# Kernel optimization log

Measured on AMD Instinct MI355X. Metric: run time of the kernel, lower is better.

## Reference

```python
import jax, jax.numpy as jnp
import numpy as np

N_RES = 768
DISTO_BINS = 64
LDDT_BINS = 50
MIN_RESOLUTION = 0.1
MAX_RESOLUTION = 3.0
W_DISTO, W_PLDDT, W_EXP = 0.3, 0.01, 0.01
CA_IDX = 1  # atom37 index of C-alpha


def setup_inputs() -> dict:
    key = jax.random.key(0)
    ks = jax.random.split(key, 6)
    B = 1
    return {
        "distogram_logits": jax.random.normal(ks[0], (B, N_RES, N_RES, DISTO_BINS), jnp.float32),
        "pseudo_beta": jax.random.normal(ks[1], (B, N_RES, 3), jnp.float32) * 10.0,
        "pseudo_beta_mask": jnp.ones((B, N_RES), jnp.float32),
        "lddt_logits": jax.random.normal(ks[2], (B, N_RES, LDDT_BINS), jnp.float32),
        "all_atom_pred_pos": jax.random.normal(ks[3], (B, N_RES, 37, 3), jnp.float32) * 10.0,
        "all_atom_positions": jax.random.normal(ks[4], (B, N_RES, 37, 3), jnp.float32) * 10.0,
        "all_atom_mask": jnp.ones((B, N_RES, 37), jnp.float32),
        "exp_resolved_logits": jax.random.normal(ks[5], (B, N_RES, 37), jnp.float32),
        "atom37_atom_exists": jnp.ones((B, N_RES, 37), jnp.float32),
        "resolution": jnp.ones((B,), jnp.float32),
    }


def _lddt(pred_pos, true_pos, mask, cutoff=15.0, eps=1e-10):
    # pred_pos/true_pos: [*, N, 3]; mask: [*, N, 1] -> per-residue lddt [*, N]
    n = mask.shape[-2]
    dmat_true = jnp.sqrt(eps + jnp.sum((true_pos[..., :, None, :] - true_pos[..., None, :, :]) ** 2, axis=-1))
    dmat_pred = jnp.sqrt(eps + jnp.sum((pred_pos[..., :, None, :] - pred_pos[..., None, :, :]) ** 2, axis=-1))
    scope = ((dmat_true < cutoff).astype(dmat_true.dtype)
             * mask * jnp.swapaxes(mask, -1, -2)
             * (1.0 - jnp.eye(n, dtype=dmat_true.dtype)))
    dist_l1 = jnp.abs(dmat_true - dmat_pred)
    score = 0.25 * ((dist_l1 < 0.5).astype(dist_l1.dtype) + (dist_l1 < 1.0)
                    + (dist_l1 < 2.0) + (dist_l1 < 4.0))
    norm = 1.0 / (eps + jnp.sum(scope, axis=-1))
    return norm * (eps + jnp.sum(scope * score, axis=-1))


def _ce_from_bins(logits, bins):
    # -sum(one_hot(bins) * log_softmax(logits)) == -log_softmax gathered at bins
    logp = jax.nn.log_softmax(logits, axis=-1)
    return -jnp.take_along_axis(logp, bins[..., None], axis=-1)[..., 0]


def _distogram_loss(logits, pseudo_beta, pseudo_beta_mask,
                    min_bin=2.3125, max_bin=21.6875, no_bins=DISTO_BINS, eps=1e-6):
    boundaries = jnp.linspace(min_bin, max_bin, no_bins - 1) ** 2
    d2 = jnp.sum((pseudo_beta[..., :, None, :] - pseudo_beta[..., None, :, :]) ** 2,
                 axis=-1, keepdims=True)  # [*, N, N, 1]
    true_bins = jnp.sum(d2 > boundaries, axis=-1).astype(jnp.int32)  # [*, N, N]
    errors = _ce_from_bins(logits, true_bins)
    sq_mask = pseudo_beta_mask[..., None] * pseudo_beta_mask[..., None, :]
    denom = eps + jnp.sum(sq_mask, axis=(-1, -2))
    mean = jnp.sum(errors * sq_mask, axis=-1) / denom[..., None]
    return jnp.mean(jnp.sum(mean, axis=-1))


def _lddt_loss(logits, all_atom_pred_pos, all_atom_positions, all_atom_mask, resolution,
               no_bins=LDDT_BINS, eps=1e-10):
    pred_ca = all_atom_pred_pos[..., CA_IDX, :]
    true_ca = all_atom_positions[..., CA_IDX, :]
    mask_ca = all_atom_mask[..., CA_IDX:CA_IDX + 1]  # [*, N, 1]
    score = jax.lax.stop_gradient(_lddt(pred_ca, true_ca, mask_ca, eps=eps))
    bin_idx = jnp.clip(jnp.floor(score * no_bins).astype(jnp.int32), 0, no_bins - 1)
    errors = _ce_from_bins(logits, bin_idx)
    m = mask_ca[..., 0]
    loss = jnp.sum(errors * m, axis=-1) / (eps + jnp.sum(m, axis=-1))
    gate = ((resolution >= MIN_RESOLUTION) & (resolution <= MAX_RESOLUTION)).astype(loss.dtype)
    return jnp.mean(loss * gate)


def _exp_resolved_loss(logits, atom37_atom_exists, all_atom_mask, resolution, eps=1e-8):
    errors = (-all_atom_mask * jax.nn.log_sigmoid(logits)
              - (1.0 - all_atom_mask) * jax.nn.log_sigmoid(-logits))
    loss = jnp.sum(errors * atom37_atom_exists, axis=-1)  # [*, N]
    loss = loss / (eps + jnp.sum(atom37_atom_exists, axis=(-1, -2)))[..., None]
    loss = jnp.sum(loss, axis=-1)
    gate = ((resolution >= MIN_RESOLUTION) & (resolution <= MAX_RESOLUTION)).astype(loss.dtype)
    return jnp.mean(loss * gate)


def reference(distogram_logits, pseudo_beta, pseudo_beta_mask, lddt_logits,
              all_atom_pred_pos, all_atom_positions, all_atom_mask,
              exp_resolved_logits, atom37_atom_exists, resolution):
    l_disto = _distogram_loss(distogram_logits, pseudo_beta, pseudo_beta_mask)
    l_plddt = _lddt_loss(lddt_logits, all_atom_pred_pos, all_atom_positions,
                         all_atom_mask, resolution)
    l_exp = _exp_resolved_loss(exp_resolved_logits, atom37_atom_exists,
                               all_atom_mask, resolution)
    return W_DISTO * l_disto + W_PLDDT * l_plddt + W_EXP * l_exp
```

## Files before the change

### kernel.cpp

```cpp
#include <hip/hip_runtime.h>
#include <math.h>

#define N_RES 768
#define DISTO_BINS 64
#define LDDT_BINS 50
#define DISTO_GRID 2048
#define EXP_GRID 64
#define NPAIRS (N_RES * N_RES)
#define NCHUNKS (NPAIRS / 4)

#define ROW_ADD_ROR(v, N)                                                     \
    v += __int_as_float(__builtin_amdgcn_update_dpp(                          \
        0, __float_as_int(v), 0x120 | (N), 0xF, 0xF, false))

__global__ __launch_bounds__(256)
void pair_meta_kernel(const float* __restrict__ pb,
                      const float* __restrict__ pbm,
                      unsigned char* __restrict__ bins,
                      float* __restrict__ wgt) {
    int p = blockIdx.x * blockDim.x + threadIdx.x;
    if (p >= NPAIRS) return;
    int i = p / N_RES;
    int j = p - i * N_RES;
    float dx = pb[3 * i + 0] - pb[3 * j + 0];
    float dy = pb[3 * i + 1] - pb[3 * j + 1];
    float dz = pb[3 * i + 2] - pb[3 * j + 2];
    float d  = sqrtf(dx * dx + dy * dy + dz * dz);
    float t  = ceilf((d - 2.3125f) * 3.2f);
    int bin  = (int)fminf(fmaxf(t, 0.f), 63.f);
    bins[p]  = (unsigned char)bin;
    wgt[p]   = pbm[i] * pbm[j];
}

__global__ __launch_bounds__(256)
void disto_partial_kernel(const float4* __restrict__ logits4,
                          const unsigned int* __restrict__ binw,
                          const float* __restrict__ wgt,
                          float* __restrict__ partial) {
    const int lane = threadIdx.x & 63;
    const int wid  = threadIdx.x >> 6;
    const int q    = lane >> 4;
    const int gl   = lane & 15;
    const int gw   = blockIdx.x * 4 + wid;
    const int nw   = DISTO_GRID * 4;

    float acc = 0.f;

#define DISTO_PROC(xv4, cc)                                                   \
    {                                                                         \
        float e = __expf(xv4.x) + __expf(xv4.y) + __expf(xv4.z) +             \
                  __expf(xv4.w);                                              \
        ROW_ADD_ROR(e, 8);                                                    \
        ROW_ADD_ROR(e, 4);                                                    \
        ROW_ADD_ROR(e, 2);                                                    \
        ROW_ADD_ROR(e, 1);                                                    \
        unsigned int bw = binw[cc];                                           \
        int bin = (int)((bw >> (q * 8)) & 63u);                               \
        float w  = wgt[(cc) * 4 + q];                                         \
        float xs = (bin & 2) ? ((bin & 1) ? xv4.w : xv4.z)                    \
                             : ((bin & 1) ? xv4.y : xv4.x);                   \
        float lg = (gl == 0) ? w * __logf(e) : 0.f;                           \
        float bt = (gl == (bin >> 2)) ? w * xs : 0.f;                         \
        acc += lg - bt;                                                       \
    }

    for (int c0 = gw; c0 < NCHUNKS; c0 += 4 * nw) {
        const int c1 = c0 + nw;
        const int c2 = c0 + 2 * nw;
        const int c3 = c0 + 3 * nw;
        float4 x0 = logits4[(size_t)c0 * 64 + lane];
        float4 x1 = (c1 < NCHUNKS) ? logits4[(size_t)c1 * 64 + lane]
                                   : make_float4(0.f, 0.f, 0.f, 0.f);
        float4 x2 = (c2 < NCHUNKS) ? logits4[(size_t)c2 * 64 + lane]
                                   : make_float4(0.f, 0.f, 0.f, 0.f);
        float4 x3 = (c3 < NCHUNKS) ? logits4[(size_t)c3 * 64 + lane]
                                   : make_float4(0.f, 0.f, 0.f, 0.f);

        DISTO_PROC(x0, c0);
        if (c1 < NCHUNKS) DISTO_PROC(x1, c1);
        if (c2 < NCHUNKS) DISTO_PROC(x2, c2);
        if (c3 < NCHUNKS) DISTO_PROC(x3, c3);
    }
#undef DISTO_PROC

    acc += __shfl_xor(acc, 1, 64);
    acc += __shfl_xor(acc, 2, 64);
    acc += __shfl_xor(acc, 4, 64);
    acc += __shfl_xor(acc, 8, 64);
    acc += __shfl_xor(acc, 16, 64);
    acc += __shfl_xor(acc, 32, 64);
    __shared__ float wsum[4];
    if (lane == 0) wsum[wid] = acc;
    __syncthreads();
    if (threadIdx.x == 0)
        partial[blockIdx.x] = wsum[0] + wsum[1] + wsum[2] + wsum[3];
}

__global__ __launch_bounds__(128)
void small_losses_kernel(const float* __restrict__ pred37,
                         const float* __restrict__ true37,
                         const float* __restrict__ mask37,
                         const float* __restrict__ lddt_logits,
                         const float* __restrict__ exl,
                         const float* __restrict__ a37ex,
                         float* __restrict__ errm,
                         float* __restrict__ expnum,
                         float* __restrict__ expden) {
    const int tid  = threadIdx.x;
    const int nthr = blockDim.x;
    __shared__ float r1[128], r2[128];

    if (blockIdx.x >= N_RES) {
        const int b = blockIdx.x - N_RES;
        const int gid = b * nthr + tid;
        const int stride = EXP_GRID * nthr;
        const int n = N_RES * 37;
        float num = 0.f, den = 0.f;
        for (int k = gid; k < n; k += stride) {
            float x  = exl[k];
            float m  = mask37[k];
            float ex = a37ex[k];
            float ax = fabsf(x);
            float sp = __logf(1.f + __expf(-ax));
            float ls  = sp + fmaxf(-x, 0.f);
            float lsn = sp + fmaxf(x, 0.f);
            float err = m * ls + (1.f - m) * lsn;
            num += err * ex;
            den += ex;
        }
        r1[tid] = num;
        r2[tid] = den;
        __syncthreads();
        for (int s = nthr >> 1; s > 0; s >>= 1) {
            if (tid < s) { r1[tid] += r1[tid + s]; r2[tid] += r2[tid + s]; }
            __syncthreads();
        }
        if (tid == 0) { expnum[b] = r1[0]; expden[b] = r2[0]; }
        return;
    }

    const int i = blockIdx.x;
    const float tix = true37[(i * 37 + 1) * 3 + 0];
    const float tiy = true37[(i * 37 + 1) * 3 + 1];
    const float tiz = true37[(i * 37 + 1) * 3 + 2];
    const float pix = pred37[(i * 37 + 1) * 3 + 0];
    const float piy = pred37[(i * 37 + 1) * 3 + 1];
    const float piz = pred37[(i * 37 + 1) * 3 + 2];
    const float mi  = mask37[i * 37 + 1];

    float scope_sum = 0.f, score_sum = 0.f;
    for (int j = tid; j < N_RES; j += nthr) {
        float mj  = mask37[j * 37 + 1];
        float dtx = tix - true37[(j * 37 + 1) * 3 + 0];
        float dty = tiy - true37[(j * 37 + 1) * 3 + 1];
        float dtz = tiz - true37[(j * 37 + 1) * 3 + 2];
        float dt  = sqrtf(1e-10f + dtx * dtx + dty * dty + dtz * dtz);
        float dpx = pix - pred37[(j * 37 + 1) * 3 + 0];
        float dpy = piy - pred37[(j * 37 + 1) * 3 + 1];
        float dpz = piz - pred37[(j * 37 + 1) * 3 + 2];
        float dp  = sqrtf(1e-10f + dpx * dpx + dpy * dpy + dpz * dpz);
        float scope = (dt < 15.f && j != i) ? (mi * mj) : 0.f;
        float l1 = fabsf(dt - dp);
        float sc = 0.25f * ((l1 < 0.5f ? 1.f : 0.f) + (l1 < 1.f ? 1.f : 0.f) +
                            (l1 < 2.f ? 1.f : 0.f) + (l1 < 4.f ? 1.f : 0.f));
        scope_sum += scope;
        score_sum += scope * sc;
    }

    r1[tid] = scope_sum;
    r2[tid] = score_sum;
    __syncthreads();
    for (int s = nthr >> 1; s > 0; s >>= 1) {
        if (tid < s) { r1[tid] += r1[tid + s]; r2[tid] += r2[tid + s]; }
        __syncthreads();
    }

    __shared__ int binS;
    if (tid == 0) {
        float lddt = (1e-10f + r2[0]) / (1e-10f + r1[0]);
        int bin = (int)floorf(lddt * (float)LDDT_BINS);
        binS = min(max(bin, 0), LDDT_BINS - 1);
    }
    __syncthreads();

    float e = (tid < LDDT_BINS) ? __expf(lddt_logits[i * LDDT_BINS + tid]) : 0.f;
    r1[tid] = e;
    __syncthreads();
    for (int s = nthr >> 1; s > 0; s >>= 1) {
        if (tid < s) r1[tid] += r1[tid + s];
        __syncthreads();
    }
    if (tid == 0) {
        float err = __logf(r1[0]) - lddt_logits[i * LDDT_BINS + binS];
        errm[i] = err * mi;
    }
}

__global__ __launch_bounds__(256)
void finalize_kernel(const float* __restrict__ partial,
                     const float* __restrict__ pbm,
                     const float* __restrict__ errm,
                     const float* __restrict__ mask37,
                     const float* __restrict__ expnum,
                     const float* __restrict__ expden,
                     const float* __restrict__ resolution,
                     float* __restrict__ out) {
    const int tid = threadIdx.x;
    const int nthr = blockDim.x;

    double sd = 0.0, sm = 0.0, se = 0.0, smca = 0.0, num = 0.0, den = 0.0;
    for (int k = tid; k < DISTO_GRID; k += nthr) sd += (double)partial[k];
    for (int k = tid; k < N_RES; k += nthr) {
        sm   += (double)pbm[k];
        se   += (double)errm[k];
        smca += (double)mask37[k * 37 + 1];
    }
    if (tid < EXP_GRID) { num = (double)expnum[tid]; den = (double)expden[tid]; }

    __shared__ double red[256];
    double vals[6] = {sd, sm, se, smca, num, den};
    double tot[6];
    for (int v = 0; v < 6; ++v) {
        red[tid] = vals[v];
        __syncthreads();
        for (int s = nthr >> 1; s > 0; s >>= 1) {
            if (tid < s) red[tid] += red[tid + s];
            __syncthreads();
        }
        tot[v] = red[0];
        __syncthreads();
    }

    if (tid == 0) {
        float res = resolution[0];
        double gate = (res >= 0.1f && res <= 3.0f) ? 1.0 : 0.0;
        double l_disto = tot[0] / (1e-6 + tot[1] * tot[1]);
        double l_plddt = tot[2] / (1e-10 + tot[3]) * gate;
        double l_exp   = tot[4] / (1e-8 + tot[5]) * gate;
        out[0] = (float)(0.3 * l_disto + 0.01 * l_plddt + 0.01 * l_exp);
    }
}

extern "C" void kernel_launch(void* const* d_in, const int* in_sizes, int n_in,
                              void* d_out, int out_size, void* d_ws, size_t ws_size,
                              hipStream_t stream) {
    const float* disto       = (const float*)d_in[0];
    const float* pb          = (const float*)d_in[1];
    const float* pbm         = (const float*)d_in[2];
    const float* lddt_logits = (const float*)d_in[3];
    const float* pred        = (const float*)d_in[4];
    const float* truep       = (const float*)d_in[5];
    const float* am          = (const float*)d_in[6];
    const float* exl         = (const float*)d_in[7];
    const float* a37         = (const float*)d_in[8];
    const float* resolution  = (const float*)d_in[9];
    float* out = (float*)d_out;

    float* ws      = (float*)d_ws;
    float* partial = ws;
    float* errm    = ws + DISTO_GRID;
    float* expnum  = errm + N_RES;
    float* expden  = expnum + EXP_GRID;
    float* wgt     = ws + 4096;
    unsigned char* bins = (unsigned char*)(wgt + NPAIRS);

    pair_meta_kernel<<<(NPAIRS + 255) / 256, 256, 0, stream>>>(pb, pbm, bins, wgt);
    disto_partial_kernel<<<DISTO_GRID, 256, 0, stream>>>(
        (const float4*)disto, (const unsigned int*)bins, wgt, partial);
    small_losses_kernel<<<N_RES + EXP_GRID, 128, 0, stream>>>(
        pred, truep, am, lddt_logits, exl, a37, errm, expnum, expden);
    finalize_kernel<<<1, 256, 0, stream>>>(partial, pbm, errm, am,
                                           expnum, expden, resolution, out);
}
```

Measured before the change: 251.6 us.

## Fuse distogram and small-loss kernels; give each wave contiguous chunks with nontemporal loads

```diff
diff --git a/kernel.cpp b/kernel.cpp
--- a/kernel.cpp
+++ b/kernel.cpp
@@ -4,10 +4,14 @@
 #define N_RES 768
 #define DISTO_BINS 64
 #define LDDT_BINS 50
-#define DISTO_GRID 2048
+#define DISTO_BLOCKS 2048
+#define LDDT_BLOCKS N_RES
 #define EXP_GRID 64
 #define NPAIRS (N_RES * N_RES)
 #define NCHUNKS (NPAIRS / 4)
+#define CHUNKS_PER_WAVE 18
+
+typedef float f32x4 __attribute__((ext_vector_type(4)));
 
 #define ROW_ADD_ROR(v, N)                                                     \
     v += __int_as_float(__builtin_amdgcn_update_dpp(                          \
@@ -33,18 +37,32 @@
 }
 
 __global__ __launch_bounds__(256)
-void disto_partial_kernel(const float4* __restrict__ logits4,
-                          const unsigned int* __restrict__ binw,
-                          const float* __restrict__ wgt,
-                          float* __restrict__ partial) {
-    const int lane = threadIdx.x & 63;
-    const int wid  = threadIdx.x >> 6;
-    const int q    = lane >> 4;
-    const int gl   = lane & 15;
-    const int gw   = blockIdx.x * 4 + wid;
-    const int nw   = DISTO_GRID * 4;
-
-    float acc = 0.f;
+void fused_main_kernel(const f32x4* __restrict__ logits4,
+                       const unsigned int* __restrict__ binw,
+                       const float* __restrict__ wgt,
+                       const float* __restrict__ pred37,
+                       const float* __restrict__ true37,
+                       const float* __restrict__ mask37,
+                       const float* __restrict__ lddt_logits,
+                       const float* __restrict__ exl,
+                       const float* __restrict__ a37ex,
+                       float* __restrict__ partial,
+                       float* __restrict__ errm,
+                       float* __restrict__ expnum,
+                       float* __restrict__ expden) {
+    __shared__ float r1[256], r2[256];
+    const int tid  = threadIdx.x;
+    const int nthr = blockDim.x;
+
+    if (blockIdx.x < DISTO_BLOCKS) {
+        const int lane = tid & 63;
+        const int wid  = tid >> 6;
+        const int q    = lane >> 4;
+        const int gl   = lane & 15;
+        const int gw   = blockIdx.x * 4 + wid;
+        const int base = gw * CHUNKS_PER_WAVE;
+
+        float acc = 0.f;
 
 #define DISTO_PROC(xv4, cc)                                                   \
     {                                                                         \
@@ -64,54 +82,45 @@
         acc += lg - bt;                                                       \
     }
 
-    for (int c0 = gw; c0 < NCHUNKS; c0 += 4 * nw) {
-        const int c1 = c0 + nw;
-        const int c2 = c0 + 2 * nw;
-        const int c3 = c0 + 3 * nw;
-        float4 x0 = logits4[(size_t)c0 * 64 + lane];
-        float4 x1 = (c1 < NCHUNKS) ? logits4[(size_t)c1 * 64 + lane]
-                                   : make_float4(0.f, 0.f, 0.f, 0.f);
-        float4 x2 = (c2 < NCHUNKS) ? logits4[(size_t)c2 * 64 + lane]
-                                   : make_float4(0.f, 0.f, 0.f, 0.f);
-        float4 x3 = (c3 < NCHUNKS) ? logits4[(size_t)c3 * 64 + lane]
-                                   : make_float4(0.f, 0.f, 0.f, 0.f);
-
-        DISTO_PROC(x0, c0);
-        if (c1 < NCHUNKS) DISTO_PROC(x1, c1);
-        if (c2 < NCHUNKS) DISTO_PROC(x2, c2);
-        if (c3 < NCHUNKS) DISTO_PROC(x3, c3);
-    }
+#pragma unroll
+        for (int t3 = 0; t3 < 3; ++t3) {
+            const int cb = base + t3 * 6;
+            f32x4 x0 = __builtin_nontemporal_load(
+                &logits4[(size_t)(cb + 0) * 64 + lane]);
+            f32x4 x1 = __builtin_nontemporal_load(
+                &logits4[(size_t)(cb + 1) * 64 + lane]);
+            f32x4 x2 = __builtin_nontemporal_load(
+                &logits4[(size_t)(cb + 2) * 64 + lane]);
+            f32x4 x3 = __builtin_nontemporal_load(
+                &logits4[(size_t)(cb + 3) * 64 + lane]);
+            f32x4 x4 = __builtin_nontemporal_load(
+                &logits4[(size_t)(cb + 4) * 64 + lane]);
+            f32x4 x5 = __builtin_nontemporal_load(
+                &logits4[(size_t)(cb + 5) * 64 + lane]);
+            DISTO_PROC(x0, cb + 0);
+            DISTO_PROC(x1, cb + 1);
+            DISTO_PROC(x2, cb + 2);
+            DISTO_PROC(x3, cb + 3);
+            DISTO_PROC(x4, cb + 4);
+            DISTO_PROC(x5, cb + 5);
+        }
 #undef DISTO_PROC
 
-    acc += __shfl_xor(acc, 1, 64);
-    acc += __shfl_xor(acc, 2, 64);
-    acc += __shfl_xor(acc, 4, 64);
-    acc += __shfl_xor(acc, 8, 64);
-    acc += __shfl_xor(acc, 16, 64);
-    acc += __shfl_xor(acc, 32, 64);
-    __shared__ float wsum[4];
-    if (lane == 0) wsum[wid] = acc;
-    __syncthreads();
-    if (threadIdx.x == 0)
-        partial[blockIdx.x] = wsum[0] + wsum[1] + wsum[2] + wsum[3];
-}
-
-__global__ __launch_bounds__(128)
-void small_losses_kernel(const float* __restrict__ pred37,
-                         const float* __restrict__ true37,
-                         const float* __restrict__ mask37,
-                         const float* __restrict__ lddt_logits,
-                         const float* __restrict__ exl,
-                         const float* __restrict__ a37ex,
-                         float* __restrict__ errm,
-                         float* __restrict__ expnum,
-                         float* __restrict__ expden) {
-    const int tid  = threadIdx.x;
-    const int nthr = blockDim.x;
-    __shared__ float r1[128], r2[128];
-
-    if (blockIdx.x >= N_RES) {
-        const int b = blockIdx.x - N_RES;
+        acc += __shfl_xor(acc, 1, 64);
+        acc += __shfl_xor(acc, 2, 64);
+        acc += __shfl_xor(acc, 4, 64);
+        acc += __shfl_xor(acc, 8, 64);
+        acc += __shfl_xor(acc, 16, 64);
+        acc += __shfl_xor(acc, 32, 64);
+        if (lane == 0) r1[wid] = acc;
+        __syncthreads();
+        if (tid == 0)
+            partial[blockIdx.x] = r1[0] + r1[1] + r1[2] + r1[3];
+        return;
+    }
+
+    if (blockIdx.x >= DISTO_BLOCKS + LDDT_BLOCKS) {
+        const int b = blockIdx.x - DISTO_BLOCKS - LDDT_BLOCKS;
         const int gid = b * nthr + tid;
         const int stride = EXP_GRID * nthr;
         const int n = N_RES * 37;
@@ -139,7 +148,7 @@
         return;
     }
 
-    const int i = blockIdx.x;
+    const int i = blockIdx.x - DISTO_BLOCKS;
     const float tix = true37[(i * 37 + 1) * 3 + 0];
     const float tiy = true37[(i * 37 + 1) * 3 + 1];
     const float tiz = true37[(i * 37 + 1) * 3 + 2];
@@ -209,7 +218,7 @@
     const int nthr = blockDim.x;
 
     double sd = 0.0, sm = 0.0, se = 0.0, smca = 0.0, num = 0.0, den = 0.0;
-    for (int k = tid; k < DISTO_GRID; k += nthr) sd += (double)partial[k];
+    for (int k = tid; k < DISTO_BLOCKS; k += nthr) sd += (double)partial[k];
     for (int k = tid; k < N_RES; k += nthr) {
         sm   += (double)pbm[k];
         se   += (double)errm[k];
@@ -258,17 +267,17 @@
 
     float* ws      = (float*)d_ws;
     float* partial = ws;
-    float* errm    = ws + DISTO_GRID;
+    float* errm    = ws + DISTO_BLOCKS;
     float* expnum  = errm + N_RES;
     float* expden  = expnum + EXP_GRID;
     float* wgt     = ws + 4096;
     unsigned char* bins = (unsigned char*)(wgt + NPAIRS);
 
     pair_meta_kernel<<<(NPAIRS + 255) / 256, 256, 0, stream>>>(pb, pbm, bins, wgt);
-    disto_partial_kernel<<<DISTO_GRID, 256, 0, stream>>>(
-        (const float4*)disto, (const unsigned int*)bins, wgt, partial);
-    small_losses_kernel<<<N_RES + EXP_GRID, 128, 0, stream>>>(
-        pred, truep, am, lddt_logits, exl, a37, errm, expnum, expden);
+    fused_main_kernel<<<DISTO_BLOCKS + LDDT_BLOCKS + EXP_GRID, 256, 0, stream>>>(
+        (const f32x4*)disto, (const unsigned int*)bins, wgt,
+        pred, truep, am, lddt_logits, exl, a37,
+        partial, errm, expnum, expden);
     finalize_kernel<<<1, 256, 0, stream>>>(partial, pbm, errm, am,
                                            expnum, expden, resolution, out);
 }
```

Result: faster. 237.2 us (-5.7%).
